# Kernel tuning notes

Measured on AMD Instinct MI355X. Metric: run time of the kernel, lower is better.

## Reference

```python
import jax, jax.numpy as jnp
import numpy as np

B, N, C_IN = 2048, 62, 512
NUM_LAYERS, H, C_OUT_PER_HEAD = 3, 8, 64


def setup_inputs() -> dict:
    key = jax.random.key(0)
    k1, k2, k3, k4 = jax.random.split(key, 4)
    x = jax.random.normal(k1, (B, N, C_IN), dtype=jnp.float32)
    L = jax.random.uniform(k2, (N, N), dtype=jnp.float32)
    W_alphas = jax.random.normal(k3, (NUM_LAYERS, H, C_IN, N), dtype=jnp.float32) * 0.05
    W = jax.random.normal(k4, (NUM_LAYERS, H, C_IN, C_OUT_PER_HEAD), dtype=jnp.float32) * 0.05
    return {"x": x, "L": L, "W_alphas": W_alphas, "W": W}


def reference(x, L, W_alphas, W):
    # x: [B, N, C]; L: [N, N]; W_alphas: [Lyr, H, C, N]; W: [Lyr, H, C, Co]
    num_layers = W_alphas.shape[0]
    n = x.shape[1]
    I = jnp.eye(n, dtype=x.dtype)
    # Chebyshev-style adjacency powers: [I, L, L@L, ...]
    adjs = [I, L]
    for _ in range(2, num_layers):
        adjs.append(adjs[-1] @ L)
    adjs = adjs[:num_layers]

    result = None
    for l in range(num_layers):
        A = adjs[l]
        A_hat = A + I
        D = A.sum(axis=-1)                      # [N]
        d_neg = jnp.where(D == 0, 0.0, 1.0 / D)  # torch: D^-1 with inf -> 0
        # attention logits per head: D_neg @ (x @ W_alphas[h]) -> [H, B, N, N]
        a = jnp.einsum('bnc,hcm->hbnm', x, W_alphas[l])
        a = d_neg[:, None] * a                   # diag(D_neg) @ M == row scaling
        a = jax.nn.leaky_relu(a, 0.01)
        a = jax.nn.softmax(a, axis=-2)           # softmax over rows (dim=-2)
        ax = jnp.einsum('nm,bmc->bnc', A_hat, x)  # A_hat @ x, shared across heads
        o = jnp.einsum('hbnm,bmc->hbnc', a, ax)
        o = jnp.einsum('hbnc,hco->hbno', o, W[l])
        o = jax.nn.relu(o)
        # concat heads along feature dim (head-major order, matching torch.cat)
        o = jnp.moveaxis(o, 0, 2).reshape(o.shape[1], n, -1)  # [B, N, H*Co]
        result = o if result is None else result + o
    return jax.nn.relu(result)
```

## Files before the change

### kernel.cpp

```cpp
#include <hip/hip_runtime.h>


using f32x4 = __attribute__((ext_vector_type(4))) float;
using s16x8 = __attribute__((ext_vector_type(8))) short;

__device__ __forceinline__ unsigned short f2bf(float f){
  unsigned int u = __builtin_bit_cast(unsigned int, f);
  u += 0x7fffu + ((u >> 16) & 1u);
  return (unsigned short)(u >> 16);
}
__device__ __forceinline__ float bf2f(unsigned short h){
  unsigned int u = ((unsigned int)h) << 16;
  return __builtin_bit_cast(float, u);
}
__device__ __forceinline__ f32x4 zf4(){ f32x4 v; v[0]=0.f; v[1]=0.f; v[2]=0.f; v[3]=0.f; return v; }

__device__ __forceinline__ void async16(const void* g, void* l){
  __builtin_amdgcn_global_load_lds((const __attribute__((address_space(1))) unsigned int*)g,
                                   (__attribute__((address_space(3))) unsigned int*)l,
                                   16, 0, 0);
}

__global__ void k_prep_adj(const float* __restrict__ L,
                           unsigned short* __restrict__ ahat,
                           float* __restrict__ dneg)
{
  __shared__ float Ls[62*62];
  __shared__ float A2s[62*62];
  const int tid = threadIdx.x;
  for (int i = tid; i < 62*62; i += 256) Ls[i] = L[i];
  __syncthreads();
  for (int i = tid; i < 62*62; i += 256){
    const int n = i / 62, m = i % 62;
    float s = 0.f;
    for (int k = 0; k < 62; ++k) s += Ls[n*62 + k] * Ls[k*62 + m];
    A2s[i] = s;
  }
  __syncthreads();
  for (int i = tid; i < 3*64*64; i += 256){
    const int l = i >> 12, r = i & 4095, n = r >> 6, m = r & 63;
    float v = 0.f;
    if (n < 62 && m < 62){
      float base = 0.f;
      if (l == 0) base = (n == m) ? 1.f : 0.f;
      else if (l == 1) base = Ls[n*62 + m];
      else base = A2s[n*62 + m];
      v = base + ((n == m) ? 1.f : 0.f);
    }
    ahat[i] = f2bf(v);
  }
  for (int i = tid; i < 3*64; i += 256){
    const int l = i >> 6, n = i & 63;
    float D = 0.f;
    if (n < 62){
      if (l == 0) D = 1.f;
      else {
        const float* src = (l == 1) ? Ls : A2s;
        for (int m = 0; m < 62; ++m) D += src[n*62 + m];
      }
    }
    dneg[i] = (D == 0.f) ? 0.f : 1.f / D;
  }
}

__global__ void k_prep_w(const float* __restrict__ Wa, const float* __restrict__ W,
                         unsigned short* __restrict__ WaT, unsigned short* __restrict__ WT)
{
  const int idx = blockIdx.x * 256 + threadIdx.x;
  if (idx < 786432){
    const int c = idx & 511, m = (idx >> 9) & 63, lh = idx >> 15;
    const float v = (m < 62) ? Wa[((size_t)lh*512 + c)*62 + m] : 0.f;
    WaT[idx] = f2bf(v);
  } else if (idx < 1572864){
    const int j = idx - 786432;
    const int c = j & 511, o = (j >> 9) & 63, lh = j >> 15;
    WT[j] = f2bf(W[((size_t)lh*512 + c)*64 + o]);
  }
}

#define LP 72

__global__ __launch_bounds__(256, 2)
void k_main(const float* __restrict__ x,
            const unsigned short* __restrict__ WaT,
            const unsigned short* __restrict__ WT,
            const unsigned short* __restrict__ ahat,
            const float* __restrict__ dneg,
            float* __restrict__ out)
{
  __shared__ __align__(16) unsigned short s_chunk[2][8192];
  __shared__ __align__(16) unsigned short s_a[64*LP];
  __shared__ __align__(16) unsigned short s_xwT[64*LP];
  __shared__ __align__(16) unsigned short s_axwT[64*LP];
  __shared__ __align__(16) float s_dneg[192];
  __shared__ __align__(16) float s_red[256];
  __shared__ __align__(16) float s_red2[256];

  const int tid  = threadIdx.x;
  const int wv   = tid >> 6;
  const int lane = tid & 63;
  const int q    = lane >> 4;
  const int m15  = lane & 15;
  const int b    = blockIdx.x;
  const int r0   = 16*wv + 4*q;

  if (tid < 192) s_dneg[tid] = dneg[tid];

  s16x8 afr[16];
  {
    const int row = 16*wv + m15;
    if (row < 62){
      const float* xp = x + ((size_t)b*62 + row)*512 + q*8;
      #pragma unroll
      for (int kk = 0; kk < 16; ++kk){
        const f32x4 f0 = *(const f32x4*)(xp + kk*32);
        const f32x4 f1 = *(const f32x4*)(xp + kk*32 + 4);
        s16x8 t;
        t[0]=(short)f2bf(f0[0]); t[1]=(short)f2bf(f0[1]); t[2]=(short)f2bf(f0[2]); t[3]=(short)f2bf(f0[3]);
        t[4]=(short)f2bf(f1[0]); t[5]=(short)f2bf(f1[1]); t[6]=(short)f2bf(f1[2]); t[7]=(short)f2bf(f1[3]);
        afr[kk] = t;
      }
    } else {
      #pragma unroll
      for (int kk = 0; kk < 16; ++kk){
        s16x8 t; t[0]=0;t[1]=0;t[2]=0;t[3]=0;t[4]=0;t[5]=0;t[6]=0;t[7]=0; afr[kk] = t;
      }
    }
  }

  #pragma unroll 1
  for (int h = 0; h < 8; ++h){
    f32x4 out_acc[4];
    #pragma unroll
    for (int ct = 0; ct < 4; ++ct) out_acc[ct] = zf4();

    #pragma unroll 1
    for (int l = 0; l < 3; ++l){
      const int lh = l*8 + h;
      const unsigned short* wa_base = WaT + (size_t)lh*32768;
      const unsigned short* wt_base = WT  + (size_t)lh*32768;

      f32x4 accL[4], accX[4];
      #pragma unroll
      for (int ct = 0; ct < 4; ++ct){ accL[ct] = zf4(); accX[ct] = zf4(); }

      #pragma unroll
      for (int kc = 0; kc < 4; ++kc){
        __syncthreads();
        #pragma unroll
        for (int tt = 0; tt < 4; ++tt){
          const int n  = 16*tt + 4*wv + q;
          const int jl = m15 ^ (n & 15);
          const size_t goff = (size_t)n*512 + (size_t)kc*128 + (size_t)jl*8;
          const int    loff = tt*2048 + wv*512 + lane*8;
          async16(wa_base + goff, &s_chunk[0][loff]);
          async16(wt_base + goff, &s_chunk[1][loff]);
        }
        __syncthreads();
        #pragma unroll
        for (int ks = 0; ks < 4; ++ks){
          const s16x8 a = afr[kc*4 + ks];
          #pragma unroll
          for (int ct = 0; ct < 4; ++ct){
            const int off = (16*ct + m15)*128 + (((4*ks + q) ^ m15) * 8);
            const s16x8 bL = *(const s16x8*)(&s_chunk[0][off]);
            const s16x8 bX = *(const s16x8*)(&s_chunk[1][off]);
            accL[ct] = __builtin_amdgcn_mfma_f32_16x16x32_bf16(a, bL, accL[ct], 0, 0, 0);
            accX[ct] = __builtin_amdgcn_mfma_f32_16x16x32_bf16(a, bX, accX[ct], 0, 0, 0);
          }
        }
      }

      {
        const f32x4 dn = *(const f32x4*)(&s_dneg[l*64 + r0]);
        #pragma unroll
        for (int ct = 0; ct < 4; ++ct){
          const int col = 16*ct + m15;
          #pragma unroll
          for (int r = 0; r < 4; ++r){
            const int n = r0 + r;
            float v = accL[ct][r] * dn[r];
            v = (v > 0.f) ? v : 0.01f*v;
            if (n >= 62) v = -1e30f;
            s_a[n*LP + col]   = f2bf(v);
            s_xwT[col*LP + n] = f2bf(accX[ct][r]);
          }
        }
      }
      __syncthreads();

      f32x4 accA[4];
      #pragma unroll
      for (int ct = 0; ct < 4; ++ct) accA[ct] = zf4();
      #pragma unroll
      for (int ks = 0; ks < 2; ++ks){
        const s16x8 aA = *(const s16x8*)(ahat + (size_t)(l*64 + 16*wv + m15)*64 + ks*32 + q*8);
        #pragma unroll
        for (int ct = 0; ct < 4; ++ct){
          const s16x8 bA = *(const s16x8*)(&s_xwT[(16*ct + m15)*LP + ks*32 + q*8]);
          accA[ct] = __builtin_amdgcn_mfma_f32_16x16x32_bf16(aA, bA, accA[ct], 0, 0, 0);
        }
      }
      #pragma unroll
      for (int ct = 0; ct < 4; ++ct){
        #pragma unroll
        for (int r = 0; r < 4; ++r)
          s_axwT[(16*ct + m15)*LP + (r0 + r)] = f2bf(accA[ct][r]);
      }

      float vsm[16];
      float mp = -3.0e38f;
      #pragma unroll
      for (int i = 0; i < 16; ++i){
        vsm[i] = bf2f(s_a[(16*wv + i)*LP + lane]);
        mp = fmaxf(mp, vsm[i]);
      }
      s_red[wv*64 + lane] = mp;
      __syncthreads();
      const float mc = fmaxf(fmaxf(s_red[lane], s_red[64 + lane]),
                             fmaxf(s_red[128 + lane], s_red[192 + lane]));
      float ev[16]; float sp = 0.f;
      #pragma unroll
      for (int i = 0; i < 16; ++i){ ev[i] = __expf(vsm[i] - mc); sp += ev[i]; }
      s_red2[wv*64 + lane] = sp;
      __syncthreads();
      const float sc = s_red2[lane] + s_red2[64 + lane] + s_red2[128 + lane] + s_red2[192 + lane];
      const float inv = 1.0f / sc;
      #pragma unroll
      for (int i = 0; i < 16; ++i)
        s_a[(16*wv + i)*LP + lane] = f2bf(ev[i] * inv);
      __syncthreads();

      f32x4 accO[4];
      #pragma unroll
      for (int ct = 0; ct < 4; ++ct) accO[ct] = zf4();
      #pragma unroll
      for (int ks = 0; ks < 2; ++ks){
        const s16x8 aO = *(const s16x8*)(&s_a[(16*wv + m15)*LP + ks*32 + q*8]);
        #pragma unroll
        for (int ct = 0; ct < 4; ++ct){
          const s16x8 bO = *(const s16x8*)(&s_axwT[(16*ct + m15)*LP + ks*32 + q*8]);
          accO[ct] = __builtin_amdgcn_mfma_f32_16x16x32_bf16(aO, bO, accO[ct], 0, 0, 0);
        }
      }
      #pragma unroll
      for (int ct = 0; ct < 4; ++ct){
        #pragma unroll
        for (int r = 0; r < 4; ++r)
          out_acc[ct][r] += fmaxf(accO[ct][r], 0.f);
      }
    }

    #pragma unroll
    for (int ct = 0; ct < 4; ++ct){
      const int col = h*64 + 16*ct + m15;
      #pragma unroll
      for (int r = 0; r < 4; ++r){
        const int n = r0 + r;
        if (n < 62)
          out[((size_t)b*62 + n)*512 + col] = fmaxf(out_acc[ct][r], 0.f);
      }
    }
  }
}

extern "C" void kernel_launch(void* const* d_in, const int* in_sizes, int n_in,
                              void* d_out, int out_size, void* d_ws, size_t ws_size,
                              hipStream_t stream)
{
  const float* x  = (const float*)d_in[0];
  const float* L  = (const float*)d_in[1];
  const float* Wa = (const float*)d_in[2];
  const float* W  = (const float*)d_in[3];
  float* out = (float*)d_out;

  char* ws = (char*)d_ws;
  unsigned short* ws_ahat = (unsigned short*)(ws);
  float*          ws_dneg = (float*)(ws + 24576);
  unsigned short* ws_WaT  = (unsigned short*)(ws + 25600);
  unsigned short* ws_WT   = (unsigned short*)(ws + 25600 + 1572864);

  k_prep_adj<<<1, 256, 0, stream>>>(L, ws_ahat, ws_dneg);
  k_prep_w<<<6144, 256, 0, stream>>>(Wa, W, ws_WaT, ws_WT);
  k_main<<<2048, 256, 0, stream>>>(x, ws_WaT, ws_WT, ws_ahat, ws_dneg, out);
}
```

Baseline: 1.046 ms.

## Switch first GEMM to 32x32 MFMA with double-buffered prefetch of fused weights

Concatenates the W_alphas and W transposes into one bf16 [lh][128][512] buffer, built by a shared-memory-tiled transpose kernel. The main kernel now uses 32x32x16 MFMA tiles (2x2 wave layout) for the x@[Wa|W] projection. Weight chunks are staged with a double-buffered asynchronous global-to-LDS pipeline, and the first chunk of the next (layer, head) is prefetched during the epilogue. This cuts barrier count and LDS read traffic per MFMA, at the cost of doubling the x fragments held in registers (32 s16x8), which raises register pressure under launch_bounds(256,2).

Measured after the change: 1.088 ms. 1.04x slower.

```diff
diff --git a/kernel.cpp b/kernel.cpp
--- a/kernel.cpp
+++ b/kernel.cpp
@@ -1,8 +1,9 @@
 #include <hip/hip_runtime.h>
 
 
-using f32x4 = __attribute__((ext_vector_type(4))) float;
-using s16x8 = __attribute__((ext_vector_type(8))) short;
+using f32x4  = __attribute__((ext_vector_type(4)))  float;
+using f32x16 = __attribute__((ext_vector_type(16))) float;
+using s16x8  = __attribute__((ext_vector_type(8)))  short;
 
 __device__ __forceinline__ unsigned short f2bf(float f){
   unsigned int u = __builtin_bit_cast(unsigned int, f);
@@ -19,6 +20,13 @@
   __builtin_amdgcn_global_load_lds((const __attribute__((address_space(1))) unsigned int*)g,
                                    (__attribute__((address_space(3))) unsigned int*)l,
                                    16, 0, 0);
+}
+
+__device__ __forceinline__ f32x16 mfma32(s16x8 a, s16x8 b, f32x16 c){
+  return __builtin_amdgcn_mfma_f32_32x32x16_bf16(a, b, c, 0, 0, 0);
+}
+__device__ __forceinline__ f32x4 mfma16(s16x8 a, s16x8 b, f32x4 c){
+  return __builtin_amdgcn_mfma_f32_16x16x32_bf16(a, b, c, 0, 0, 0);
 }
 
 __global__ void k_prep_adj(const float* __restrict__ L,
@@ -64,26 +72,43 @@
 }
 
 __global__ void k_prep_w(const float* __restrict__ Wa, const float* __restrict__ W,
-                         unsigned short* __restrict__ WaT, unsigned short* __restrict__ WT)
-{
-  const int idx = blockIdx.x * 256 + threadIdx.x;
-  if (idx < 786432){
-    const int c = idx & 511, m = (idx >> 9) & 63, lh = idx >> 15;
-    const float v = (m < 62) ? Wa[((size_t)lh*512 + c)*62 + m] : 0.f;
-    WaT[idx] = f2bf(v);
-  } else if (idx < 1572864){
-    const int j = idx - 786432;
-    const int c = j & 511, o = (j >> 9) & 63, lh = j >> 15;
-    WT[j] = f2bf(W[((size_t)lh*512 + c)*64 + o]);
+                         unsigned short* __restrict__ WC)
+{
+  __shared__ float t0[64*65];
+  __shared__ float t1[64*65];
+  const int lh = blockIdx.x >> 3;
+  const int c0 = (blockIdx.x & 7) * 64;
+  for (int i = threadIdx.x; i < 64*64; i += 256){
+    const int cc = i >> 6, n = i & 63;
+    t0[n*65 + cc] = (n < 62) ? Wa[((size_t)lh*512 + c0 + cc)*62 + n] : 0.f;
+    t1[n*65 + cc] = W[((size_t)lh*512 + c0 + cc)*64 + n];
+  }
+  __syncthreads();
+  for (int i = threadIdx.x; i < 64*64; i += 256){
+    const int n = i >> 6, cc = i & 63;
+    WC[((size_t)lh*128 + n)*512 + c0 + cc]      = f2bf(t0[n*65 + cc]);
+    WC[((size_t)lh*128 + 64 + n)*512 + c0 + cc] = f2bf(t1[n*65 + cc]);
   }
 }
 
 #define LP 72
+
+__device__ __forceinline__ void stage_chunk(const unsigned short* __restrict__ wcb, int kc,
+                                            unsigned short* dst, int wv, int lane)
+{
+  const int l3 = lane >> 3, kb0 = lane & 7;
+  #pragma unroll
+  for (int t = 0; t < 4; ++t){
+    const int n  = wv*32 + t*8 + l3;
+    const int kb = kb0 ^ (n & 7);
+    async16(wcb + (size_t)n*512 + kc*64 + kb*8,
+            dst + wv*2048 + t*512 + lane*8);
+  }
+}
 
 __global__ __launch_bounds__(256, 2)
 void k_main(const float* __restrict__ x,
-            const unsigned short* __restrict__ WaT,
-            const unsigned short* __restrict__ WT,
+            const unsigned short* __restrict__ WC,
             const unsigned short* __restrict__ ahat,
             const float* __restrict__ dneg,
             float* __restrict__ out)
@@ -101,32 +126,43 @@
   const int lane = tid & 63;
   const int q    = lane >> 4;
   const int m15  = lane & 15;
+  const int l31  = lane & 31;
+  const int lh5  = lane >> 5;
+  const int wr   = wv >> 1;
+  const int wc   = wv & 1;
   const int b    = blockIdx.x;
   const int r0   = 16*wv + 4*q;
 
   if (tid < 192) s_dneg[tid] = dneg[tid];
 
-  s16x8 afr[16];
+  stage_chunk(WC, 0, &s_chunk[0][0], wv, lane);
+
+  s16x8 afr[32];
   {
-    const int row = 16*wv + m15;
+    const int row = 32*wr + l31;
     if (row < 62){
-      const float* xp = x + ((size_t)b*62 + row)*512 + q*8;
-      #pragma unroll
-      for (int kk = 0; kk < 16; ++kk){
-        const f32x4 f0 = *(const f32x4*)(xp + kk*32);
-        const f32x4 f1 = *(const f32x4*)(xp + kk*32 + 4);
+      const float* xp = x + ((size_t)b*62 + row)*512 + 8*lh5;
+      #pragma unroll
+      for (int i = 0; i < 32; ++i){
+        const f32x4 f0 = *(const f32x4*)(xp + i*16);
+        const f32x4 f1 = *(const f32x4*)(xp + i*16 + 4);
         s16x8 t;
         t[0]=(short)f2bf(f0[0]); t[1]=(short)f2bf(f0[1]); t[2]=(short)f2bf(f0[2]); t[3]=(short)f2bf(f0[3]);
         t[4]=(short)f2bf(f1[0]); t[5]=(short)f2bf(f1[1]); t[6]=(short)f2bf(f1[2]); t[7]=(short)f2bf(f1[3]);
-        afr[kk] = t;
+        afr[i] = t;
       }
     } else {
       #pragma unroll
-      for (int kk = 0; kk < 16; ++kk){
-        s16x8 t; t[0]=0;t[1]=0;t[2]=0;t[3]=0;t[4]=0;t[5]=0;t[6]=0;t[7]=0; afr[kk] = t;
-      }
-    }
-  }
+      for (int i = 0; i < 32; ++i){
+        s16x8 t; t[0]=0;t[1]=0;t[2]=0;t[3]=0;t[4]=0;t[5]=0;t[6]=0;t[7]=0; afr[i] = t;
+      }
+    }
+  }
+  __syncthreads();
+
+  const int nA = wc*32 + l31;
+  const int nX = nA + 64;
+  const int n7 = nA & 7;
 
   #pragma unroll 1
   for (int h = 0; h < 8; ++h){
@@ -137,54 +173,46 @@
     #pragma unroll 1
     for (int l = 0; l < 3; ++l){
       const int lh = l*8 + h;
-      const unsigned short* wa_base = WaT + (size_t)lh*32768;
-      const unsigned short* wt_base = WT  + (size_t)lh*32768;
-
-      f32x4 accL[4], accX[4];
-      #pragma unroll
-      for (int ct = 0; ct < 4; ++ct){ accL[ct] = zf4(); accX[ct] = zf4(); }
-
-      #pragma unroll
-      for (int kc = 0; kc < 4; ++kc){
-        __syncthreads();
-        #pragma unroll
-        for (int tt = 0; tt < 4; ++tt){
-          const int n  = 16*tt + 4*wv + q;
-          const int jl = m15 ^ (n & 15);
-          const size_t goff = (size_t)n*512 + (size_t)kc*128 + (size_t)jl*8;
-          const int    loff = tt*2048 + wv*512 + lane*8;
-          async16(wa_base + goff, &s_chunk[0][loff]);
-          async16(wt_base + goff, &s_chunk[1][loff]);
+      int ln = l + 1, hn = h;
+      if (ln == 3){ ln = 0; hn = (h + 1) & 7; }
+      const int lh_next = ln*8 + hn;
+      const unsigned short* wcb  = WC + (size_t)lh*65536;
+      const unsigned short* wcbn = WC + (size_t)lh_next*65536;
+
+      f32x16 accL, accX;
+      #pragma unroll
+      for (int i = 0; i < 16; ++i){ accL[i] = 0.f; accX[i] = 0.f; }
+
+      #pragma unroll
+      for (int ck = 0; ck < 8; ++ck){
+        if (ck < 7) stage_chunk(wcb, ck+1, &s_chunk[(ck+1)&1][0], wv, lane);
+        const unsigned short* sc = &s_chunk[ck&1][0];
+        #pragma unroll
+        for (int ks = 0; ks < 4; ++ks){
+          const s16x8 a  = afr[ck*4 + ks];
+          const int   kb = 2*ks + lh5;
+          const s16x8 bL = *(const s16x8*)(sc + nA*64 + ((kb ^ n7) * 8));
+          const s16x8 bX = *(const s16x8*)(sc + nX*64 + ((kb ^ n7) * 8));
+          accL = mfma32(a, bL, accL);
+          accX = mfma32(a, bX, accX);
         }
         __syncthreads();
-        #pragma unroll
-        for (int ks = 0; ks < 4; ++ks){
-          const s16x8 a = afr[kc*4 + ks];
-          #pragma unroll
-          for (int ct = 0; ct < 4; ++ct){
-            const int off = (16*ct + m15)*128 + (((4*ks + q) ^ m15) * 8);
-            const s16x8 bL = *(const s16x8*)(&s_chunk[0][off]);
-            const s16x8 bX = *(const s16x8*)(&s_chunk[1][off]);
-            accL[ct] = __builtin_amdgcn_mfma_f32_16x16x32_bf16(a, bL, accL[ct], 0, 0, 0);
-            accX[ct] = __builtin_amdgcn_mfma_f32_16x16x32_bf16(a, bX, accX[ct], 0, 0, 0);
-          }
-        }
-      }
-
-      {
-        const f32x4 dn = *(const f32x4*)(&s_dneg[l*64 + r0]);
-        #pragma unroll
-        for (int ct = 0; ct < 4; ++ct){
-          const int col = 16*ct + m15;
-          #pragma unroll
-          for (int r = 0; r < 4; ++r){
-            const int n = r0 + r;
-            float v = accL[ct][r] * dn[r];
-            v = (v > 0.f) ? v : 0.01f*v;
-            if (n >= 62) v = -1e30f;
-            s_a[n*LP + col]   = f2bf(v);
-            s_xwT[col*LP + n] = f2bf(accX[ct][r]);
-          }
+      }
+
+      stage_chunk(wcbn, 0, &s_chunk[0][0], wv, lane);
+
+      #pragma unroll
+      for (int g = 0; g < 4; ++g){
+        const f32x4 dn = *(const f32x4*)(&s_dneg[l*64 + 32*wr + 8*g + 4*lh5]);
+        #pragma unroll
+        for (int rr = 0; rr < 4; ++rr){
+          const int row = 8*g + 4*lh5 + rr;
+          const int n   = 32*wr + row;
+          float v = accL[4*g + rr] * dn[rr];
+          v = (v > 0.f) ? v : 0.01f*v;
+          if (n >= 62) v = -1e30f;
+          s_a[n*LP + 32*wc + l31]   = f2bf(v);
+          s_xwT[(32*wc + l31)*LP + n] = f2bf(accX[4*g + rr]);
         }
       }
       __syncthreads();
@@ -198,7 +226,7 @@
         #pragma unroll
         for (int ct = 0; ct < 4; ++ct){
           const s16x8 bA = *(const s16x8*)(&s_xwT[(16*ct + m15)*LP + ks*32 + q*8]);
-          accA[ct] = __builtin_amdgcn_mfma_f32_16x16x32_bf16(aA, bA, accA[ct], 0, 0, 0);
+          accA[ct] = mfma16(aA, bA, accA[ct]);
         }
       }
       #pragma unroll
@@ -224,8 +252,8 @@
       for (int i = 0; i < 16; ++i){ ev[i] = __expf(vsm[i] - mc); sp += ev[i]; }
       s_red2[wv*64 + lane] = sp;
       __syncthreads();
-      const float sc = s_red2[lane] + s_red2[64 + lane] + s_red2[128 + lane] + s_red2[192 + lane];
-      const float inv = 1.0f / sc;
+      const float sc2 = s_red2[lane] + s_red2[64 + lane] + s_red2[128 + lane] + s_red2[192 + lane];
+      const float inv = 1.0f / sc2;
       #pragma unroll
       for (int i = 0; i < 16; ++i)
         s_a[(16*wv + i)*LP + lane] = f2bf(ev[i] * inv);
@@ -240,7 +268,7 @@
         #pragma unroll
         for (int ct = 0; ct < 4; ++ct){
           const s16x8 bO = *(const s16x8*)(&s_axwT[(16*ct + m15)*LP + ks*32 + q*8]);
-          accO[ct] = __builtin_amdgcn_mfma_f32_16x16x32_bf16(aO, bO, accO[ct], 0, 0, 0);
+          accO[ct] = mfma16(aO, bO, accO[ct]);
         }
       }
       #pragma unroll
@@ -277,10 +305,9 @@
   char* ws = (char*)d_ws;
   unsigned short* ws_ahat = (unsigned short*)(ws);
   float*          ws_dneg = (float*)(ws + 24576);
-  unsigned short* ws_WaT  = (unsigned short*)(ws + 25600);
-  unsigned short* ws_WT   = (unsigned short*)(ws + 25600 + 1572864);
+  unsigned short* ws_WC   = (unsigned short*)(ws + 25600);
 
   k_prep_adj<<<1, 256, 0, stream>>>(L, ws_ahat, ws_dneg);
-  k_prep_w<<<6144, 256, 0, stream>>>(Wa, W, ws_WaT, ws_WT);
-  k_main<<<2048, 256, 0, stream>>>(x, ws_WaT, ws_WT, ws_ahat, ws_dneg, out);
-}
+  k_prep_w<<<192, 256, 0, stream>>>(Wa, W, ws_WC);
+  k_main<<<2048, 256, 0, stream>>>(x, ws_WC, ws_ahat, ws_dneg, out);
+}
```
